# Performance work log

Measured on AMD Instinct MI355X. Metric: run time of the kernel, lower is better.

The kernel has to match this reference:

```python
import jax, jax.numpy as jnp
import numpy as np

ALPHA = 0.1


def rois_to_rois(f1, f2, N, A):
    # f1, f2: [A*N*K, C, 1, 1]
    M, C = f1.shape[0], f1.shape[1]
    K = M // (A * N)
    a = f1.reshape(A, N, K, C).transpose(1, 0, 3, 2)  # [N,A,C,K] (query/value)
    b = f2.reshape(A, N, K, C).transpose(1, 0, 3, 2)  # [N,A,C,K] (key/residual)
    # outer product a_i * b_j per (n, anchor, channel), softmax over i (torch dim=1 of [G,K,K])
    rel = a[..., :, None] * b[..., None, :]            # [N,A,C,Ki,Kj]
    w = jax.nn.softmax(rel, axis=-2)
    out = b + jnp.einsum('nacij,naci->nacj', w, a)     # [N,A,C,Kj]
    # torch: reshape->[N,A,C,K,1], permute [1,0,3,2,4] -> [A,N,K,C,1] -> [M,C,1,1]
    return out.transpose(1, 0, 3, 2).reshape(M, C, 1, 1)


def bilinear_sample(feat, px, py):
    # feat [C,H,W]; px, py [A,F,F] pixel coords -> [C,A,F,F]
    H, W = feat.shape[1], feat.shape[2]
    x0 = jnp.floor(px)
    y0 = jnp.floor(py)
    wx = px - x0
    wy = py - y0
    x0i = jnp.clip(x0.astype(jnp.int32), 0, W - 1)
    x1i = jnp.clip(x0i + 1, 0, W - 1)
    y0i = jnp.clip(y0.astype(jnp.int32), 0, H - 1)
    y1i = jnp.clip(y0i + 1, 0, H - 1)
    v00 = feat[:, y0i, x0i]
    v01 = feat[:, y0i, x1i]
    v10 = feat[:, y1i, x0i]
    v11 = feat[:, y1i, x1i]
    return (v00 * (1 - wx) * (1 - wy) + v01 * wx * (1 - wy)
            + v10 * (1 - wx) * wy + v11 * wx * wy)


def reference(ori_feature_shape, rois_feature_a, feature_b, rois_feature_c, W_reg, b_reg):
    N, C, H, W = feature_b.shape
    A = W_reg.shape[0]
    bs = W_reg.shape[2]
    F = H // bs
    K = F * F
    reg = jax.lax.conv_general_dilated(
        feature_b, W_reg, (bs, bs), 'VALID',
        dimension_numbers=('NCHW', 'OIHW', 'NCHW')) + b_reg[None, :, None, None]  # [N,A,F,F]
    # block centers (matches r = arange(0.5*(bs-1), ..., step=bs))
    r = 0.5 * (bs - 1) + bs * jnp.arange(F, dtype=feature_b.dtype)
    xc = jnp.broadcast_to(r[None, :], (F, F))   # x varies along last dim
    yc = xc.T
    cx = xc[None, None] + ALPHA * bs * jnp.tanh(reg)
    cy = yc[None, None] + ALPHA * bs * jnp.tanh(reg)
    samp = jax.vmap(bilinear_sample)(feature_b, cx, cy)       # [N,C,A,F,F]
    rois_feature_b = samp.transpose(2, 0, 3, 4, 1).reshape(A * N * K, C, 1, 1)
    out = rois_to_rois(rois_feature_a, rois_feature_b, N, A)
    out = rois_to_rois(out, rois_feature_c, N, A)
    return out


def setup_inputs() -> dict:
    key = jax.random.key(0)
    k1, k2, k3, k4 = jax.random.split(key, 4)
    N, C, H, W = 8, 256, 64, 64
    A, bs = 9, 8
    F = H // bs
    K = F * F
    M = A * N * K
    return {
        'ori_feature_shape': jnp.array([N, C, H, W], dtype=jnp.int32),
        'rois_feature_a': jax.random.normal(k1, (M, C, 1, 1), dtype=jnp.float32),
        'feature_b': jax.random.normal(k2, (N, C, H, W), dtype=jnp.float32),
        'rois_feature_c': jax.random.normal(k3, (M, C, 1, 1), dtype=jnp.float32),
        'W_reg': jax.random.normal(k4, (A, C, bs, bs), dtype=jnp.float32) * 0.01,
        'b_reg': jnp.zeros((A,), dtype=jnp.float32),
    }
```

## Files before the change

### kernel.cpp

```cpp
#include <hip/hip_runtime.h>

constexpr int N_ = 8, C_ = 256, H_ = 64, W_ = 64, A_ = 9, F_ = 8, K_ = 64;
constexpr int M_ = A_ * N_ * K_;
constexpr int NPOS = 512;
constexpr int PSTRIDE = 9 * 32;
constexpr int NJOBS2 = A_ * N_ * (C_ / 8);
#define ALPHA_BS 0.8f
#define L2E 1.442695040888963f

typedef float f32x2 __attribute__((ext_vector_type(2)));

__global__ __launch_bounds__(256) void kA(const float* __restrict__ feat,
                                          const float* __restrict__ Wreg,
                                          float* __restrict__ partials) {
    const int bi = blockIdx.x;
    const int chunk = bi & 7;
    const int g = (bi >> 3) & 63;
    const int pair = bi >> 9;
    const int n = g >> 3, gy = g & 7;
    const int t = threadIdx.x;
    const int lane = t & 63, wid = t >> 6;
    const int r = t & 7;
    const int c = chunk * 32 + (t >> 3);

    const float* wp = Wreg + chunk * 2048 + t * 8;
    float4 w0[9], w1[9];
#pragma unroll
    for (int a = 0; a < 9; ++a) {
        w0[a] = *(const float4*)(wp + (size_t)a * 16384);
        w1[a] = *(const float4*)(wp + (size_t)a * 16384 + 4);
    }
    const float* frow = feat + (((size_t)n * C_ + c) * H_ + gy * 8 + r) * W_;
#pragma unroll
    for (int i = 0; i < 2; ++i) {
        const int gx = pair * 2 + i;
        const float4 f0 = *(const float4*)(frow + gx * 8);
        const float4 f1 = *(const float4*)(frow + gx * 8 + 4);
        float* pp = partials + (size_t)(g * 8 + gx) * PSTRIDE + chunk * 4 + wid;
#pragma unroll
        for (int a = 0; a < 9; ++a) {
            float s = f0.x * w0[a].x + f0.y * w0[a].y + f0.z * w0[a].z + f0.w * w0[a].w;
            s = fmaf(f1.x, w1[a].x, s);
            s = fmaf(f1.y, w1[a].y, s);
            s = fmaf(f1.z, w1[a].z, s);
            s = fmaf(f1.w, w1[a].w, s);
            s += __shfl_xor(s, 1, 64);
            s += __shfl_xor(s, 2, 64);
            s += __shfl_xor(s, 4, 64);
            s += __shfl_xor(s, 8, 64);
            s += __shfl_xor(s, 16, 64);
            s += __shfl_xor(s, 32, 64);
            if (lane == 0) pp[a * 32] = s;
        }
    }
}

__global__ __launch_bounds__(256, 4) void kB(const float* __restrict__ feat,
                                             const float* __restrict__ partials,
                                             const float* __restrict__ breg,
                                             float* __restrict__ rfb) {
    __shared__ float tile[128][65];
    __shared__ float sW[9][4];
    __shared__ int   sI[9][4];

    const int bi = blockIdx.x;
    const int u  = (bi & 7) * 128 + (bi >> 3);
    const int b = u >> 1, half = u & 1;
    const int n = b >> 6, gy = (b >> 3) & 7, gx = b & 7;
    const int t = threadIdx.x;

    if (t < 72) {
        const int a = t >> 3, q = t & 7;
        const float4 v = *(const float4*)(partials + (size_t)b * PSTRIDE + a * 32 + q * 4);
        float s = v.x + v.y + v.z + v.w;
        s += __shfl_xor(s, 1, 64);
        s += __shfl_xor(s, 2, 64);
        s += __shfl_xor(s, 4, 64);
        if (q == 0) {
            float rr  = s + breg[a];
            float off = ALPHA_BS * tanhf(rr);
            float cx = 3.5f + 8.0f * gx + off;
            float cy = 3.5f + 8.0f * gy + off;
            float x0f = floorf(cx), y0f = floorf(cy);
            float wx = cx - x0f, wy = cy - y0f;
            int x0 = min(max((int)x0f, 0), W_ - 1);
            int x1 = min(x0 + 1, W_ - 1);
            int y0 = min(max((int)y0f, 0), H_ - 1);
            int y1 = min(y0 + 1, H_ - 1);
            int lx0 = x0 - gx * 8, lx1 = x1 - gx * 8;
            int ly0 = y0 - gy * 8, ly1 = y1 - gy * 8;
            sI[a][0] = ly0 * 8 + lx0;
            sI[a][1] = ly0 * 8 + lx1;
            sI[a][2] = ly1 * 8 + lx0;
            sI[a][3] = ly1 * 8 + lx1;
            sW[a][0] = (1.f - wx) * (1.f - wy);
            sW[a][1] = wx * (1.f - wy);
            sW[a][2] = (1.f - wx) * wy;
            sW[a][3] = wx * wy;
        }
    }

    const float* fb = feat + (((size_t)n * C_ + half * 128) * H_ + gy * 8) * W_ + gx * 8;
#pragma unroll
    for (int it = 0; it < 8; ++it) {
        int q = t + 256 * it;
        int c = q >> 4, rr = (q >> 1) & 7, h = q & 1;
        float4 v = *(const float4*)(fb + ((size_t)c * H_ + rr) * W_ + h * 4);
        int e = rr * 8 + h * 4;
        tile[c][e + 0] = v.x;
        tile[c][e + 1] = v.y;
        tile[c][e + 2] = v.z;
        tile[c][e + 3] = v.w;
    }
    __syncthreads();

    const int kidx = gy * 8 + gx;
    const int cl = t & 127;
    const int p = t >> 7;
    for (int a = p ? 5 : 0; a < (p ? 9 : 5); ++a) {
        float v = sW[a][0] * tile[cl][sI[a][0]] + sW[a][1] * tile[cl][sI[a][1]] +
                  sW[a][2] * tile[cl][sI[a][2]] + sW[a][3] * tile[cl][sI[a][3]];
        rfb[((size_t)(a * N_ + n) * K_ + kidx) * C_ + half * 128 + cl] = v;
    }
}

__global__ __launch_bounds__(256, 4) void kRf(const float* __restrict__ rois_a,
                                              const float* __restrict__ rfb,
                                              const float* __restrict__ rois_c,
                                              float* __restrict__ out) {
    __shared__ __align__(16) float sa[64][10];
    __shared__ __align__(16) float sb[64][10];
    __shared__ __align__(16) float sc[64][10];

    const int bi = blockIdx.x;
    const int j  = (bi & 7) * 288 + (bi >> 3);
    const int na = j >> 5;
    const int cb = (j & 31) * 8;
    const int t = threadIdx.x, lane = t & 63, w = t >> 6;
    const int cp = 2 * w;
    const size_t base = (size_t)na * 64;

    float rc[2];
#pragma unroll
    for (int k = 0; k < 2; ++k) {
        int idx = t + 256 * k;
        int i = idx >> 3, cc = idx & 7;
        sa[i][cc] = rois_a[(base + i) * 256 + cb + cc];
        sb[i][cc] = rfb[(base + i) * 256 + cb + cc];
        rc[k]     = rois_c[(base + i) * 256 + cb + cc];
    }
    __syncthreads();

    const f32x2 a1 = *(const f32x2*)&sa[lane][cp];
    const f32x2 b1 = *(const f32x2*)&sb[lane][cp];
    f32x2 o1;
    {
        float mx0 = a1.x, mn0 = a1.x, mx1 = a1.y, mn1 = a1.y;
#pragma unroll
        for (int s = 32; s; s >>= 1) {
            mx0 = fmaxf(mx0, __shfl_xor(mx0, s, 64));
            mn0 = fminf(mn0, __shfl_xor(mn0, s, 64));
            mx1 = fmaxf(mx1, __shfl_xor(mx1, s, 64));
            mn1 = fminf(mn1, __shfl_xor(mn1, s, 64));
        }
        f32x2 m;
        m.x = b1.x > 0.f ? b1.x * mx0 : b1.x * mn0;
        m.y = b1.y > 0.f ? b1.y * mx1 : b1.y * mn1;
        const f32x2 bl2 = b1 * L2E;
        const f32x2 ml2 = -m * L2E;
        f32x2 den = {0.f, 0.f}, num = {0.f, 0.f};
#pragma unroll 16
        for (int i = 0; i < 64; ++i) {
            const f32x2 av = *(const f32x2*)&sa[i][cp];
            f32x2 eg = av * bl2 + ml2;
            f32x2 e;
            e.x = __builtin_amdgcn_exp2f(eg.x);
            e.y = __builtin_amdgcn_exp2f(eg.y);
            den += e;
            num += e * av;
        }
        o1 = b1 + num / den;
    }
    __syncthreads();

    *(f32x2*)&sa[lane][cp] = o1;
#pragma unroll
    for (int k = 0; k < 2; ++k) {
        int idx = t + 256 * k;
        sb[idx >> 3][idx & 7] = rc[k];
    }
    __syncthreads();

    {
        const f32x2 b2 = *(const f32x2*)&sb[lane][cp];
        float mx0 = o1.x, mn0 = o1.x, mx1 = o1.y, mn1 = o1.y;
#pragma unroll
        for (int s = 32; s; s >>= 1) {
            mx0 = fmaxf(mx0, __shfl_xor(mx0, s, 64));
            mn0 = fminf(mn0, __shfl_xor(mn0, s, 64));
            mx1 = fmaxf(mx1, __shfl_xor(mx1, s, 64));
            mn1 = fminf(mn1, __shfl_xor(mn1, s, 64));
        }
        f32x2 m;
        m.x = b2.x > 0.f ? b2.x * mx0 : b2.x * mn0;
        m.y = b2.y > 0.f ? b2.y * mx1 : b2.y * mn1;
        const f32x2 bl2 = b2 * L2E;
        const f32x2 ml2 = -m * L2E;
        f32x2 den = {0.f, 0.f}, num = {0.f, 0.f};
#pragma unroll 16
        for (int i = 0; i < 64; ++i) {
            const f32x2 av = *(const f32x2*)&sa[i][cp];
            f32x2 eg = av * bl2 + ml2;
            f32x2 e;
            e.x = __builtin_amdgcn_exp2f(eg.x);
            e.y = __builtin_amdgcn_exp2f(eg.y);
            den += e;
            num += e * av;
        }
        *(f32x2*)&sc[lane][cp] = b2 + num / den;
    }
    __syncthreads();

#pragma unroll
    for (int k = 0; k < 2; ++k) {
        int idx = t + 256 * k;
        int i = idx >> 3, cc = idx & 7;
        out[(base + i) * 256 + cb + cc] = sc[i][cc];
    }
}

extern "C" void kernel_launch(void* const* d_in, const int* in_sizes, int n_in,
                              void* d_out, int out_size, void* d_ws, size_t ws_size,
                              hipStream_t stream) {
    const float* rois_a = (const float*)d_in[1];
    const float* feat   = (const float*)d_in[2];
    const float* rois_c = (const float*)d_in[3];
    const float* Wreg   = (const float*)d_in[4];
    const float* breg   = (const float*)d_in[5];
    float* out = (float*)d_out;
    float* partials = (float*)d_ws;
    float* rfb      = (float*)d_ws + (size_t)NPOS * PSTRIDE;

    kA<<<dim3(NPOS * 4), dim3(256), 0, stream>>>(feat, Wreg, partials);
    kB<<<dim3(NPOS * 2), dim3(256), 0, stream>>>(feat, partials, breg, rfb);
    kRf<<<dim3(NJOBS2), dim3(256), 0, stream>>>(rois_a, rfb, rois_c, out);
}
```

Baseline: 53.38 us.

## Fuse bilinear sampling kernel into the rois-to-rois attention kernel

Removes the separate sampling kernel and its intermediate rfb buffer. Each attention block now reduces the regression partials, computes the tanh offsets for its 64 positions, and bilinearly samples the feature map directly from global memory into shared memory. This saves one launch and a write/read round trip of the sampled features. In exchange it does scattered, uncoalesced gathers from the feature map and repeats the offset computation in every channel block. It also lowers the softmax loop unroll from 16 to 8.

```diff
diff --git a/kernel.cpp b/kernel.cpp
--- a/kernel.cpp
+++ b/kernel.cpp
@@ -1,10 +1,9 @@
 #include <hip/hip_runtime.h>
 
 constexpr int N_ = 8, C_ = 256, H_ = 64, W_ = 64, A_ = 9, F_ = 8, K_ = 64;
-constexpr int M_ = A_ * N_ * K_;
 constexpr int NPOS = 512;
 constexpr int PSTRIDE = 9 * 32;
-constexpr int NJOBS2 = A_ * N_ * (C_ / 8);
+constexpr int NJOBS = A_ * N_ * (C_ / 8);
 #define ALPHA_BS 0.8f
 #define L2E 1.442695040888963f
 
@@ -55,90 +54,38 @@
     }
 }
 
-__global__ __launch_bounds__(256, 4) void kB(const float* __restrict__ feat,
-                                             const float* __restrict__ partials,
-                                             const float* __restrict__ breg,
-                                             float* __restrict__ rfb) {
-    __shared__ float tile[128][65];
-    __shared__ float sW[9][4];
-    __shared__ int   sI[9][4];
-
-    const int bi = blockIdx.x;
-    const int u  = (bi & 7) * 128 + (bi >> 3);
-    const int b = u >> 1, half = u & 1;
-    const int n = b >> 6, gy = (b >> 3) & 7, gx = b & 7;
-    const int t = threadIdx.x;
-
-    if (t < 72) {
-        const int a = t >> 3, q = t & 7;
-        const float4 v = *(const float4*)(partials + (size_t)b * PSTRIDE + a * 32 + q * 4);
-        float s = v.x + v.y + v.z + v.w;
-        s += __shfl_xor(s, 1, 64);
-        s += __shfl_xor(s, 2, 64);
-        s += __shfl_xor(s, 4, 64);
-        if (q == 0) {
-            float rr  = s + breg[a];
-            float off = ALPHA_BS * tanhf(rr);
-            float cx = 3.5f + 8.0f * gx + off;
-            float cy = 3.5f + 8.0f * gy + off;
-            float x0f = floorf(cx), y0f = floorf(cy);
-            float wx = cx - x0f, wy = cy - y0f;
-            int x0 = min(max((int)x0f, 0), W_ - 1);
-            int x1 = min(x0 + 1, W_ - 1);
-            int y0 = min(max((int)y0f, 0), H_ - 1);
-            int y1 = min(y0 + 1, H_ - 1);
-            int lx0 = x0 - gx * 8, lx1 = x1 - gx * 8;
-            int ly0 = y0 - gy * 8, ly1 = y1 - gy * 8;
-            sI[a][0] = ly0 * 8 + lx0;
-            sI[a][1] = ly0 * 8 + lx1;
-            sI[a][2] = ly1 * 8 + lx0;
-            sI[a][3] = ly1 * 8 + lx1;
-            sW[a][0] = (1.f - wx) * (1.f - wy);
-            sW[a][1] = wx * (1.f - wy);
-            sW[a][2] = (1.f - wx) * wy;
-            sW[a][3] = wx * wy;
-        }
-    }
-
-    const float* fb = feat + (((size_t)n * C_ + half * 128) * H_ + gy * 8) * W_ + gx * 8;
-#pragma unroll
-    for (int it = 0; it < 8; ++it) {
-        int q = t + 256 * it;
-        int c = q >> 4, rr = (q >> 1) & 7, h = q & 1;
-        float4 v = *(const float4*)(fb + ((size_t)c * H_ + rr) * W_ + h * 4);
-        int e = rr * 8 + h * 4;
-        tile[c][e + 0] = v.x;
-        tile[c][e + 1] = v.y;
-        tile[c][e + 2] = v.z;
-        tile[c][e + 3] = v.w;
-    }
-    __syncthreads();
-
-    const int kidx = gy * 8 + gx;
-    const int cl = t & 127;
-    const int p = t >> 7;
-    for (int a = p ? 5 : 0; a < (p ? 9 : 5); ++a) {
-        float v = sW[a][0] * tile[cl][sI[a][0]] + sW[a][1] * tile[cl][sI[a][1]] +
-                  sW[a][2] * tile[cl][sI[a][2]] + sW[a][3] * tile[cl][sI[a][3]];
-        rfb[((size_t)(a * N_ + n) * K_ + kidx) * C_ + half * 128 + cl] = v;
-    }
-}
-
-__global__ __launch_bounds__(256, 4) void kRf(const float* __restrict__ rois_a,
-                                              const float* __restrict__ rfb,
-                                              const float* __restrict__ rois_c,
-                                              float* __restrict__ out) {
+__global__ __launch_bounds__(256, 4) void kRfB(const float* __restrict__ rois_a,
+                                               const float* __restrict__ feat,
+                                               const float* __restrict__ partials,
+                                               const float* __restrict__ breg,
+                                               const float* __restrict__ rois_c,
+                                               float* __restrict__ out) {
     __shared__ __align__(16) float sa[64][10];
     __shared__ __align__(16) float sb[64][10];
     __shared__ __align__(16) float sc[64][10];
+    __shared__ float soff[64];
 
     const int bi = blockIdx.x;
-    const int j  = (bi & 7) * 288 + (bi >> 3);
-    const int na = j >> 5;
-    const int cb = (j & 31) * 8;
+    const int n  = bi & 7;
+    const int r9 = bi >> 3;
+    const int a9 = r9 >> 5;
+    const int cb = (r9 & 31) * 8;
+    const int na = a9 * N_ + n;
     const int t = threadIdx.x, lane = t & 63, w = t >> 6;
     const int cp = 2 * w;
     const size_t base = (size_t)na * 64;
+
+    {
+        const int q = t & 3, jj = t >> 2;
+        const float* pp = partials +
+            (size_t)((n * 8 + (jj >> 3)) * 8 + (jj & 7)) * PSTRIDE + a9 * 32 + q * 8;
+        const float4 v0 = *(const float4*)pp;
+        const float4 v1 = *(const float4*)(pp + 4);
+        float s = v0.x + v0.y + v0.z + v0.w + v1.x + v1.y + v1.z + v1.w;
+        s += __shfl_xor(s, 1, 64);
+        s += __shfl_xor(s, 2, 64);
+        if (q == 0) soff[jj] = ALPHA_BS * tanhf(s + breg[a9]);
+    }
 
     float rc[2];
 #pragma unroll
@@ -146,8 +93,29 @@
         int idx = t + 256 * k;
         int i = idx >> 3, cc = idx & 7;
         sa[i][cc] = rois_a[(base + i) * 256 + cb + cc];
-        sb[i][cc] = rfb[(base + i) * 256 + cb + cc];
         rc[k]     = rois_c[(base + i) * 256 + cb + cc];
+    }
+    __syncthreads();
+
+    {
+        const int j = t & 63, cg = t >> 6;
+        const int gy = j >> 3, gx = j & 7;
+        const float off = soff[j];
+        const float cx = 3.5f + 8.0f * gx + off;
+        const float cy = 3.5f + 8.0f * gy + off;
+        const float x0f = floorf(cx), y0f = floorf(cy);
+        const float wx = cx - x0f, wy = cy - y0f;
+        const int x0 = (int)x0f, y0 = (int)y0f;
+        const float w00 = (1.f - wx) * (1.f - wy), w01 = wx * (1.f - wy);
+        const float w10 = (1.f - wx) * wy,         w11 = wx * wy;
+#pragma unroll
+        for (int k = 0; k < 2; ++k) {
+            const int c = cb + cg * 2 + k;
+            const float* fp = feat + (((size_t)n * C_ + c) * H_ + y0) * W_ + x0;
+            const float v00 = fp[0], v01 = fp[1];
+            const float v10 = fp[W_], v11 = fp[W_ + 1];
+            sb[j][cg * 2 + k] = w00 * v00 + w01 * v01 + w10 * v10 + w11 * v11;
+        }
     }
     __syncthreads();
 
@@ -169,7 +137,7 @@
         const f32x2 bl2 = b1 * L2E;
         const f32x2 ml2 = -m * L2E;
         f32x2 den = {0.f, 0.f}, num = {0.f, 0.f};
-#pragma unroll 16
+#pragma unroll 8
         for (int i = 0; i < 64; ++i) {
             const f32x2 av = *(const f32x2*)&sa[i][cp];
             f32x2 eg = av * bl2 + ml2;
@@ -207,7 +175,7 @@
         const f32x2 bl2 = b2 * L2E;
         const f32x2 ml2 = -m * L2E;
         f32x2 den = {0.f, 0.f}, num = {0.f, 0.f};
-#pragma unroll 16
+#pragma unroll 8
         for (int i = 0; i < 64; ++i) {
             const f32x2 av = *(const f32x2*)&sa[i][cp];
             f32x2 eg = av * bl2 + ml2;
@@ -239,9 +207,8 @@
     const float* breg   = (const float*)d_in[5];
     float* out = (float*)d_out;
     float* partials = (float*)d_ws;
-    float* rfb      = (float*)d_ws + (size_t)NPOS * PSTRIDE;
 
     kA<<<dim3(NPOS * 4), dim3(256), 0, stream>>>(feat, Wreg, partials);
-    kB<<<dim3(NPOS * 2), dim3(256), 0, stream>>>(feat, partials, breg, rfb);
-    kRf<<<dim3(NJOBS2), dim3(256), 0, stream>>>(rois_a, rfb, rois_c, out);
+    kRfB<<<dim3(NJOBS), dim3(256), 0, stream>>>(rois_a, feat, partials, breg,
+                                                rois_c, out);
 }
```

Result: faster. 47.32 us (-11.4%).
